# Kernel tuning notes

Hardware: AMD Instinct MI355X
Metric: run time of the kernel (lower is better)

Reference implementation:

```python
import jax, jax.numpy as jnp
import numpy as np

S = 32        # window size along the 'time' (intra-patch) axis
C = 32        # channels
P = 4         # patch_size; T = P**3 = 64 = 2*S


def setup_inputs() -> dict:
    key = jax.random.key(0)
    k1, k2, k3 = jax.random.split(key, 3)
    x = jax.random.normal(k1, (2, C, 96, 96, 96), dtype=jnp.float32)
    # nn.Linear(S*C, S*C): weight (out,in), bias (out,)
    W = jax.random.normal(k2, (S * C, S * C), dtype=jnp.float32) / np.float32(np.sqrt(S * C))
    b = jax.random.normal(k3, (S * C,), dtype=jnp.float32) * 0.01
    return {"x": x, "W": W, "b": b}


def reference(x, W, b):
    B, Cc, H, Wd, D = x.shape
    Hp, Wp, Dp = H // P, Wd // P, D // P
    T = P ** 3  # intra-patch token count
    # (B,C,H,W,D) -> (B,C,T,H',W',D') -> (B,H',W',D',T,C)
    xr = x.reshape(B, Cc, T, Hp, Wp, Dp).transpose(0, 3, 4, 5, 2, 1)
    # shift_window: circular roll along T by S//2
    xr = jnp.roll(xr, S // 2, axis=4)
    # group T into windows of S, dense linear over S*C
    xg = xr.reshape(B, Hp, Wp, Dp, T // S, S * Cc)
    y = jnp.einsum('bhwdgk,ok->bhwdgo', xg, W) + b
    # roll back by -(S//2)
    y = jnp.roll(y.reshape(B, Hp, Wp, Dp, T, Cc), -(S // 2), axis=4)
    # (B,H',W',D',T,C) -> (B,C,T,H',W',D') -> (B,C,H,W,D)
    out = y.transpose(0, 5, 4, 1, 2, 3).reshape(B, Cc, H, Wd, D)
    return out
```

## Files before the change

kernel.cpp:

```cpp
#include <hip/hip_runtime.h>


#define NSPAT 884736
#define QQ    13824
#define MTOT  55296
#define KK    1024

#define NBLK_XC 27648
#define NBLK_W  256

typedef __attribute__((ext_vector_type(4))) float f32x4;
typedef __attribute__((ext_vector_type(8))) short bf16x8;

__device__ __forceinline__ short f2bf(float f) {
  unsigned u = __builtin_bit_cast(unsigned, f);
  u += 0x7fff + ((u >> 16) & 1);
  return (short)(u >> 16);
}

__device__ __forceinline__ void async16(short* lds, const short* g) {
  __builtin_amdgcn_global_load_lds(
      (const __attribute__((address_space(1))) unsigned*)g,
      (__attribute__((address_space(3))) unsigned*)lds, 16, 0, 0);
}

__global__ __launch_bounds__(256)
void convert_pre(const float* __restrict__ x, const float* __restrict__ Wm,
                 short* __restrict__ Abf, short* __restrict__ Wbf) {
  const int bid = blockIdx.x;
  const int tid = threadIdx.x;
  if (bid < NBLK_XC) {
    const int kb  = bid & 15;
    const int mt  = bid >> 4;
    const int mi  = tid & 31;
    const int m   = mt * 32 + mi;
    const int seg = mt / 432;
    const int q   = m - seg * 13824;
    const int bb  = seg >> 1;
    const int g   = seg & 1;
    const int k0t = kb * 64 + (tid >> 5) * 8;
    const int j   = k0t >> 5;
    const int tsrc = ((g << 5) + j + 48) & 63;
    const int cb  = k0t & 31;
    const float* src = x + (size_t)bb * 32 * NSPAT + (size_t)tsrc * QQ + q;
    bf16x8 f;
#pragma unroll
    for (int t = 0; t < 8; t++)
      f[t] = f2bf(src[(size_t)(cb + t) * NSPAT]);
    *(bf16x8*)(Abf + (size_t)m * KK + k0t) = f;
  } else {
    const int base = (bid - NBLK_XC) * 4096 + tid * 16;
#pragma unroll
    for (int h = 0; h < 2; h++) {
      const f32x4 a = *(const f32x4*)(Wm + base + h * 8);
      const f32x4 b = *(const f32x4*)(Wm + base + h * 8 + 4);
      bf16x8 f;
#pragma unroll
      for (int t = 0; t < 4; t++) { f[t] = f2bf(a[t]); f[t + 4] = f2bf(b[t]); }
      *(bf16x8*)(Wbf + base + h * 8) = f;
    }
  }
}

__global__ __launch_bounds__(256, 2)
void swin_mfma(const short* __restrict__ A, const short* __restrict__ Bw,
               const float* __restrict__ bias, float* __restrict__ out) {
  __shared__ __align__(16) short As[128 * 64];
  __shared__ __align__(16) short Bs[128 * 64];

  const int bid = blockIdx.x;
  const int nt  = bid & 7;
  const int mt  = bid >> 3;
  const int seg = mt / 108;
  const int q0  = (mt - seg * 108) * 128;
  const int bb  = seg >> 1;
  const int g   = seg & 1;
  const int m0  = mt * 128;
  const int n0  = nt * 128;

  const int tid  = threadIdx.x;
  const int wv   = tid >> 6;
  const int lane = tid & 63;
  const int wr   = wv >> 1;
  const int wc   = wv & 1;
  const int lm   = lane & 15;
  const int quad = lane >> 4;

  const int srow  = wv * 32 + (lane >> 3);
  const int skoff = (lane & 7) * 8;
  const short* aG = A  + (size_t)(m0 + srow) * KK + skoff;
  const short* bG = Bw + (size_t)(n0 + srow) * KK + skoff;
  short* aL = As + wv * 32 * 64;
  short* bL = Bs + wv * 32 * 64;

  f32x4 acc[4][4];
#pragma unroll
  for (int i = 0; i < 4; i++)
#pragma unroll
    for (int jj = 0; jj < 4; jj++) {
      f32x4 z = {0.f, 0.f, 0.f, 0.f};
      acc[i][jj] = z;
    }

  for (int kt = 0; kt < 16; kt++) {
    const int kof = kt * 64;
#pragma unroll
    for (int is = 0; is < 4; is++) {
      async16(aL + is * 8 * 64, aG + kof + (size_t)is * 8 * KK);
      async16(bL + is * 8 * 64, bG + kof + (size_t)is * 8 * KK);
    }
    __syncthreads();
#pragma unroll
    for (int ks = 0; ks < 2; ks++) {
      bf16x8 af[4], bfr[4];
#pragma unroll
      for (int i = 0; i < 4; i++)
        af[i] = *(const bf16x8*)(As + (wr * 64 + i * 16 + lm) * 64 + ks * 32 + quad * 8);
#pragma unroll
      for (int jj = 0; jj < 4; jj++)
        bfr[jj] = *(const bf16x8*)(Bs + (wc * 64 + jj * 16 + lm) * 64 + ks * 32 + quad * 8);
#pragma unroll
      for (int i = 0; i < 4; i++)
#pragma unroll
        for (int jj = 0; jj < 4; jj++)
          acc[i][jj] = __builtin_amdgcn_mfma_f32_16x16x32_bf16(af[i], bfr[jj], acc[i][jj], 0, 0, 0);
    }
    __syncthreads();
  }

  float* ob = out + (size_t)bb * 32 * NSPAT;
#pragma unroll
  for (int jj = 0; jj < 4; jj++) {
    const int o  = n0 + wc * 64 + jj * 16 + lm;
    const float bv = bias[o];
    const int so = o >> 5;
    const int cc = o & 31;
    const int tt = ((g << 5) + so + 48) & 63;
    float* orow = ob + (size_t)cc * NSPAT + (size_t)tt * QQ + q0;
#pragma unroll
    for (int i = 0; i < 4; i++) {
      const int mb = wr * 64 + i * 16 + quad * 4;
      f32x4 v = acc[i][jj];
      v += bv;
      *(f32x4*)(orow + mb) = v;
    }
  }
}

__global__ __launch_bounds__(256, 2)
void swin_gemm(const float* __restrict__ x, const float* __restrict__ Wm,
               const float* __restrict__ bias, float* __restrict__ out) {
  const int bid = blockIdx.x;
  const int nt  = bid & 7;
  const int mt  = bid >> 3;
  const int seg = mt / 108;
  const int q0  = (mt - seg * 108) * 128;
  const int bb  = seg >> 1;
  const int g   = seg & 1;

  const int tid  = threadIdx.x;
  const int wv   = tid >> 6;
  const int wr   = wv >> 1;
  const int wc   = wv & 1;
  const int lane = tid & 63;
  const int lm   = lane & 15;
  const int quad = lane >> 4;

  const int n0 = nt * 128 + wc * 64;

  int aoff[4];
#pragma unroll
  for (int i = 0; i < 4; i++)
    aoff[i] = (quad * 8) * NSPAT + q0 + wr * 64 + i * 16 + lm;

  const float* wptr[4];
#pragma unroll
  for (int j = 0; j < 4; j++)
    wptr[j] = Wm + (size_t)(n0 + j * 16 + lm) * 1024 + quad * 8;

  f32x4 acc[4][4];
#pragma unroll
  for (int i = 0; i < 4; i++)
#pragma unroll
    for (int j = 0; j < 4; j++) {
      f32x4 z = {0.f, 0.f, 0.f, 0.f};
      acc[i][j] = z;
    }

  const float* xb = x + (size_t)bb * 32 * NSPAT;

  for (int kc = 0; kc < 32; kc++) {
    const int t_src = ((g << 5) + kc + 48) & 63;
    const float* xs = xb + (size_t)t_src * QQ;

    bf16x8 af[4];
#pragma unroll
    for (int i = 0; i < 4; i++) {
      float v[8];
#pragma unroll
      for (int t = 0; t < 8; t++)
        v[t] = xs[aoff[i] + t * NSPAT];
      bf16x8 f;
#pragma unroll
      for (int t = 0; t < 8; t++) f[t] = f2bf(v[t]);
      af[i] = f;
    }

    bf16x8 bfr[4];
#pragma unroll
    for (int j = 0; j < 4; j++) {
      const float* wp = wptr[j] + kc * 32;
      const f32x4 w0 = *(const f32x4*)(wp);
      const f32x4 w1 = *(const f32x4*)(wp + 4);
      bf16x8 f;
#pragma unroll
      for (int t = 0; t < 4; t++) { f[t] = f2bf(w0[t]); f[t + 4] = f2bf(w1[t]); }
      bfr[j] = f;
    }

#pragma unroll
    for (int i = 0; i < 4; i++)
#pragma unroll
      for (int j = 0; j < 4; j++)
        acc[i][j] = __builtin_amdgcn_mfma_f32_16x16x32_bf16(af[i], bfr[j], acc[i][j], 0, 0, 0);
  }

  float* ob = out + (size_t)bb * 32 * NSPAT;
#pragma unroll
  for (int j = 0; j < 4; j++) {
    const int o  = n0 + j * 16 + lm;
    const float bv = bias[o];
    const int so = o >> 5;
    const int cc = o & 31;
    const int tt = ((g << 5) + so + 48) & 63;
    float* orow = ob + (size_t)cc * NSPAT + (size_t)tt * QQ + q0;
#pragma unroll
    for (int i = 0; i < 4; i++) {
      const int mb = wr * 64 + i * 16 + quad * 4;
      f32x4 v = acc[i][j];
      v += bv;
      *(f32x4*)(orow + mb) = v;
    }
  }
}

extern "C" void kernel_launch(void* const* d_in, const int* in_sizes, int n_in,
                              void* d_out, int out_size, void* d_ws, size_t ws_size,
                              hipStream_t stream) {
  const float* x    = (const float*)d_in[0];
  const float* Wm   = (const float*)d_in[1];
  const float* bias = (const float*)d_in[2];
  float* out        = (float*)d_out;

  const size_t need = (size_t)MTOT * KK * 2 + (size_t)KK * KK * 2;
  if (ws_size >= need) {
    short* Abf = (short*)d_ws;
    short* Wbf = (short*)d_ws + (size_t)MTOT * KK;
    convert_pre<<<dim3(NBLK_XC + NBLK_W), dim3(256), 0, stream>>>(x, Wm, Abf, Wbf);
    swin_mfma<<<dim3(432 * 8), dim3(256), 0, stream>>>(Abf, Wbf, bias, out);
  } else {
    swin_gemm<<<dim3(432 * 8), dim3(256), 0, stream>>>(x, Wm, bias, out);
  }
}
```

Measured before the change: 553.9 us.

## Pre-tile bf16 operands into contiguous 128x64 tiles and remap GEMM block order

The conversion kernel now reads x with 16-byte vector loads and writes A and W in bf16 as contiguous 128x64 K-tiles, so each GEMM tile load is one linear 16 KB chunk instead of 128 strided rows. The GEMM's global-to-LDS copies index into these tiles directly. Block IDs are also remapped so consecutive blocks share the same N tile and walk across M tiles. The aim is cheaper, coalesced conversion and simpler tile fetches with better L2 locality. The trade-off is a workspace layout that only this kernel understands.

```diff
diff --git a/kernel.cpp b/kernel.cpp
--- a/kernel.cpp
+++ b/kernel.cpp
@@ -5,9 +5,10 @@
 #define QQ    13824
 #define MTOT  55296
 #define KK    1024
-
-#define NBLK_XC 27648
-#define NBLK_W  256
+#define TS    8192
+
+#define NBLK_A  6912
+#define NBLK_W  128
 
 typedef __attribute__((ext_vector_type(4))) float f32x4;
 typedef __attribute__((ext_vector_type(8))) short bf16x8;
@@ -29,35 +30,50 @@
                  short* __restrict__ Abf, short* __restrict__ Wbf) {
   const int bid = blockIdx.x;
   const int tid = threadIdx.x;
-  if (bid < NBLK_XC) {
-    const int kb  = bid & 15;
-    const int mt  = bid >> 4;
-    const int mi  = tid & 31;
-    const int m   = mt * 32 + mi;
-    const int seg = mt / 432;
-    const int q   = m - seg * 13824;
+  if (bid < NBLK_A) {
+    const int mt = bid >> 4;
+    const int kt = bid & 15;
+    const int seg = mt / 108;
+    const int q0  = (mt - seg * 108) * 128;
     const int bb  = seg >> 1;
     const int g   = seg & 1;
-    const int k0t = kb * 64 + (tid >> 5) * 8;
-    const int j   = k0t >> 5;
-    const int tsrc = ((g << 5) + j + 48) & 63;
-    const int cb  = k0t & 31;
-    const float* src = x + (size_t)bb * 32 * NSPAT + (size_t)tsrc * QQ + q;
-    bf16x8 f;
-#pragma unroll
-    for (int t = 0; t < 8; t++)
-      f[t] = f2bf(src[(size_t)(cb + t) * NSPAT]);
-    *(bf16x8*)(Abf + (size_t)m * KK + k0t) = f;
+
+    const int rg = tid >> 3;
+    const int oc = tid & 7;
+    const int jp    = oc >> 2;
+    const int cbase = (oc & 3) * 8;
+    const int tsrc  = ((g << 5) + kt * 2 + jp + 48) & 63;
+
+    const float* base = x + ((size_t)bb * 32 + cbase) * NSPAT
+                          + (size_t)tsrc * QQ + q0 + rg * 4;
+    bf16x8 o[4];
+#pragma unroll
+    for (int tt = 0; tt < 8; tt++) {
+      const f32x4 v = *(const f32x4*)(base + (size_t)tt * NSPAT);
+#pragma unroll
+      for (int r = 0; r < 4; r++) o[r][tt] = f2bf(v[r]);
+    }
+    short* dst = Abf + (size_t)(mt * 16 + kt) * TS + (rg * 4) * 64 + oc * 8;
+#pragma unroll
+    for (int r = 0; r < 4; r++)
+      *(bf16x8*)(dst + r * 64) = o[r];
   } else {
-    const int base = (bid - NBLK_XC) * 4096 + tid * 16;
-#pragma unroll
-    for (int h = 0; h < 2; h++) {
-      const f32x4 a = *(const f32x4*)(Wm + base + h * 8);
-      const f32x4 b = *(const f32x4*)(Wm + base + h * 8 + 4);
+    const int wb = bid - NBLK_A;
+    const int nt = wb >> 4;
+    const int kt = wb & 15;
+    const int n0 = nt * 128;
+#pragma unroll
+    for (int it = 0; it < 4; it++) {
+      const int idx = it * 256 + tid;
+      const int row = idx >> 3;
+      const int oc2 = idx & 7;
+      const float* wsrc = Wm + (size_t)(n0 + row) * 1024 + kt * 64 + oc2 * 8;
+      const f32x4 a = *(const f32x4*)(wsrc);
+      const f32x4 b = *(const f32x4*)(wsrc + 4);
       bf16x8 f;
 #pragma unroll
       for (int t = 0; t < 4; t++) { f[t] = f2bf(a[t]); f[t + 4] = f2bf(b[t]); }
-      *(bf16x8*)(Wbf + base + h * 8) = f;
+      *(bf16x8*)(Wbf + (size_t)wb * TS + row * 64 + oc2 * 8) = f;
     }
   }
 }
@@ -68,14 +84,14 @@
   __shared__ __align__(16) short As[128 * 64];
   __shared__ __align__(16) short Bs[128 * 64];
 
-  const int bid = blockIdx.x;
-  const int nt  = bid & 7;
-  const int mt  = bid >> 3;
+  const int b0 = blockIdx.x;
+  const int logical = (b0 & 7) * 432 + (b0 >> 3);
+  const int nt = logical & 7;
+  const int mt = logical >> 3;
   const int seg = mt / 108;
   const int q0  = (mt - seg * 108) * 128;
   const int bb  = seg >> 1;
   const int g   = seg & 1;
-  const int m0  = mt * 128;
   const int n0  = nt * 128;
 
   const int tid  = threadIdx.x;
@@ -86,10 +102,8 @@
   const int lm   = lane & 15;
   const int quad = lane >> 4;
 
-  const int srow  = wv * 32 + (lane >> 3);
-  const int skoff = (lane & 7) * 8;
-  const short* aG = A  + (size_t)(m0 + srow) * KK + skoff;
-  const short* bG = Bw + (size_t)(n0 + srow) * KK + skoff;
+  const short* aT = A  + (size_t)mt * 16 * TS + wv * 2048 + lane * 8;
+  const short* bT = Bw + (size_t)nt * 16 * TS + wv * 2048 + lane * 8;
   short* aL = As + wv * 32 * 64;
   short* bL = Bs + wv * 32 * 64;
 
@@ -103,11 +117,11 @@
     }
 
   for (int kt = 0; kt < 16; kt++) {
-    const int kof = kt * 64;
+    const size_t kof = (size_t)kt * TS;
 #pragma unroll
     for (int is = 0; is < 4; is++) {
-      async16(aL + is * 8 * 64, aG + kof + (size_t)is * 8 * KK);
-      async16(bL + is * 8 * 64, bG + kof + (size_t)is * 8 * KK);
+      async16(aL + is * 8 * 64, aT + kof + is * 512);
+      async16(bL + is * 8 * 64, bT + kof + is * 512);
     }
     __syncthreads();
 #pragma unroll
@@ -256,7 +270,7 @@
   if (ws_size >= need) {
     short* Abf = (short*)d_ws;
     short* Wbf = (short*)d_ws + (size_t)MTOT * KK;
-    convert_pre<<<dim3(NBLK_XC + NBLK_W), dim3(256), 0, stream>>>(x, Wm, Abf, Wbf);
+    convert_pre<<<dim3(NBLK_A + NBLK_W), dim3(256), 0, stream>>>(x, Wm, Abf, Wbf);
     swin_mfma<<<dim3(432 * 8), dim3(256), 0, stream>>>(Abf, Wbf, bias, out);
   } else {
     swin_gemm<<<dim3(432 * 8), dim3(256), 0, stream>>>(x, Wm, bias, out);
```

After: 530.4 us. 4.2% less time.
